# Kernel optimization log

Measured on AMD Instinct MI355X. Metric: run time of the kernel, lower is better.

## Reference

```python
import jax, jax.numpy as jnp
import numpy as np

B, C, H, W = 16, 192, 64, 64
L = 256           # number of quantization levels (len(sos.unique_values))
EXTREMA = 10.0    # codebook support roughly [-extrema, extrema]


def setup_inputs() -> dict:
    key = jax.random.key(0)
    k1, k2, k3 = jax.random.split(key, 3)
    inputs = jax.random.normal(k1, (B, C, H, W), dtype=jnp.float32) * 3.0
    means = jax.random.normal(k2, (B, C, H, W), dtype=jnp.float32)
    # sorted codebook of unique quantizer output values (sos.unique_values)
    raw = jax.random.uniform(k3, (L,), dtype=jnp.float32,
                             minval=-EXTREMA, maxval=EXTREMA)
    unique_values = jnp.sort(raw)
    return {"inputs": inputs, "means": means, "unique_values": unique_values}


def _nearest_symbols(v, unique_values):
    # Parallel binary search over the sorted codebook; equivalent to the
    # original per-element argmin(|keys - x|) in transform_map.
    L_ = unique_values.shape[0]
    idx = jnp.searchsorted(unique_values, v)          # in [0, L]
    idx = jnp.clip(idx, 1, L_ - 1)
    left = unique_values[idx - 1]
    right = unique_values[idx]
    # on ties, argmin picks the lower index -> use <=
    return jnp.where(jnp.abs(v - left) <= jnp.abs(v - right), idx - 1, idx)


def reference(inputs, means, unique_values):
    # quantize(mode='symbols'): subtract means, snap to nearest codebook
    # value, map value -> integer symbol via the sorted codebook.
    v = inputs - means
    symbols = _nearest_symbols(v, unique_values)      # int32 [B,C,H,W]
    # dequantize: symbol -> float codebook value (map_cdf_sos), add means.
    dequant = unique_values[symbols] + means          # float32 [B,C,H,W]
    return dequant, symbols
```

## Files before the change

### kernel.cpp

```cpp
#include <hip/hip_runtime.h>
#include <math.h>


#define LVL 256

__device__ __forceinline__ int lb_bj(const int* s_bj, int x) {
    int lo = 0, hi = LVL;
    #pragma unroll
    for (int s = 0; s < 8; ++s) {
        int mid = (lo + hi) >> 1;
        bool r = (s_bj[mid] < x);
        lo = r ? mid + 1 : lo;
        hi = r ? hi : mid;
    }
    return lo;
}

__global__ __launch_bounds__(256) void agc_build(
    const float* __restrict__ uv, float* __restrict__ ws, int NB)
{
    __shared__ float s_uv[LVL];
    __shared__ float s_mid[LVL];
    __shared__ int   s_bj[LVL];
    int tid = threadIdx.x;
    s_uv[tid] = uv[tid];
    __syncthreads();
    float mid = (tid < LVL - 1) ? 0.5f * (s_uv[tid] + s_uv[tid + 1]) : INFINITY;
    s_mid[tid] = mid;
    __syncthreads();
    float lo = s_mid[0], hi = s_mid[LVL - 2];
    float scale = (float)NB / (hi - lo);
    float f = (mid - lo) * scale;
    f = fminf(fmaxf(f, 0.0f), (float)(NB - 1));
    s_bj[tid] = (tid < LVL - 1) ? (int)f : 0x7fffffff;
    __syncthreads();

    if (blockIdx.x == 0) {
        float4 p;
        p.x = s_mid[tid];
        p.y = s_uv[tid];
        p.z = (tid < LVL - 1) ? s_uv[tid + 1] : s_uv[LVL - 1];
        p.w = 0.0f;
        ((float4*)ws)[tid] = p;
        if (tid == 0) { ws[1024] = lo; ws[1025] = scale; }
    }

    unsigned short* T = (unsigned short*)((char*)ws + 4608);
    int stride = gridDim.x * blockDim.x;
    for (int m = blockIdx.x * blockDim.x + tid; m < NB; m += stride) {
        int l0 = lb_bj(s_bj, m);
        int l1 = lb_bj(s_bj, m + 1);
        int cnt = l1 - l0;
        int base = l0 > 255 ? 255 : l0;
        int c = cnt > 2 ? 2 : cnt;
        T[m] = (unsigned short)(base | (c << 8));
    }
}

__device__ __forceinline__ int lb_mid(const float4* s_pack, float v) {
    int lo = 0, hi = LVL;
    #pragma unroll
    for (int s = 0; s < 8; ++s) {
        int mid = (lo + hi) >> 1;
        bool r = (s_pack[mid].x < v);
        lo = r ? mid + 1 : lo;
        hi = r ? hi : mid;
    }
    return lo;
}

__device__ __forceinline__ void agc_one4(
    const float4& a, const float4& b, const float4* s_pack,
    const unsigned short* __restrict__ T, float lo, float scale, float fNBm1,
    float4& dq, float4& sy)
{
    float v[4]  = {a.x - b.x, a.y - b.y, a.z - b.z, a.w - b.w};
    float me[4] = {b.x, b.y, b.z, b.w};
    float dqs[4], sys[4];
    int slow = 0;
    #pragma unroll
    for (int k = 0; k < 4; ++k) {
        float f = (v[k] - lo) * scale;
        f = fminf(fmaxf(f, 0.0f), fNBm1);
        int e = T[(int)f];
        int base = e & 255;
        int c = e >> 8;
        float4 p = s_pack[base];
        bool take = (c == 1) && (p.x < v[k]);
        sys[k] = (float)(base + (take ? 1 : 0));
        dqs[k] = (take ? p.z : p.y) + me[k];
        slow |= (c == 2) << k;
    }
    if (slow) {
        #pragma unroll
        for (int k = 0; k < 4; ++k) if ((slow >> k) & 1) {
            int s = lb_mid(s_pack, v[k]);
            sys[k] = (float)s;
            dqs[k] = s_pack[s].y + me[k];
        }
    }
    dq = make_float4(dqs[0], dqs[1], dqs[2], dqs[3]);
    sy = make_float4(sys[0], sys[1], sys[2], sys[3]);
}

__global__ __launch_bounds__(256) void agc_quant(
    const float* __restrict__ inputs, const float* __restrict__ means,
    const float* __restrict__ ws, const unsigned short* __restrict__ T,
    float* __restrict__ out_deq, float* __restrict__ out_sym,
    int n4, int n, int NB)
{
    __shared__ float4 s_pack[LVL];
    int tid = threadIdx.x;
    s_pack[tid] = ((const float4*)ws)[tid];
    float lo = ws[1024], scale = ws[1025];
    __syncthreads();

    const float4* in4 = (const float4*)inputs;
    const float4* mn4 = (const float4*)means;
    float4* dq4 = (float4*)out_deq;
    float4* sy4 = (float4*)out_sym;
    float fNBm1 = (float)(NB - 1);

    int i0 = blockIdx.x * 512 + tid;
    int i1 = i0 + 256;

    if (i1 < n4) {
        float4 a0 = in4[i0], b0 = mn4[i0], a1 = in4[i1], b1 = mn4[i1];
        float4 dq0, sy0, dq1, sy1;
        agc_one4(a0, b0, s_pack, T, lo, scale, fNBm1, dq0, sy0);
        agc_one4(a1, b1, s_pack, T, lo, scale, fNBm1, dq1, sy1);
        dq4[i0] = dq0; dq4[i1] = dq1;
        sy4[i0] = sy0; sy4[i1] = sy1;
    } else {
        if (i0 < n4) {
            float4 a = in4[i0], b = mn4[i0], dq, sy;
            agc_one4(a, b, s_pack, T, lo, scale, fNBm1, dq, sy);
            dq4[i0] = dq; sy4[i0] = sy;
        }
        if (i1 < n4) {
            float4 a = in4[i1], b = mn4[i1], dq, sy;
            agc_one4(a, b, s_pack, T, lo, scale, fNBm1, dq, sy);
            dq4[i1] = dq; sy4[i1] = sy;
        }
    }

    if (blockIdx.x == 0 && tid == 0) {
        for (int j = n4 * 4; j < n; ++j) {
            float m = means[j];
            float v = inputs[j] - m;
            int s = lb_mid(s_pack, v);
            out_sym[j] = (float)s;
            out_deq[j] = s_pack[s].y + m;
        }
    }
}

extern "C" void kernel_launch(void* const* d_in, const int* in_sizes, int n_in,
                              void* d_out, int out_size, void* d_ws, size_t ws_size,
                              hipStream_t stream) {
    const float* inputs = (const float*)d_in[0];
    const float* means  = (const float*)d_in[1];
    const float* uv     = (const float*)d_in[2];

    int n  = in_sizes[0];
    int n4 = n / 4;

    float* out     = (float*)d_out;
    float* out_deq = out;
    float* out_sym = out + n;
    float* ws      = (float*)d_ws;

    long long avail = (long long)ws_size > 4608 ? ((long long)ws_size - 4608) / 2 : 1024;
    int NB = 1024;
    while ((long long)NB * 2 <= avail && NB < 32768) NB <<= 1;
    unsigned short* T = (unsigned short*)((char*)d_ws + 4608);

    agc_build<<<32, 256, 0, stream>>>(uv, ws, NB);

    int blocks = (n4 + 511) / 512;
    agc_quant<<<blocks, 256, 0, stream>>>(
        inputs, means, ws, T, out_deq, out_sym, n4, n, NB);
}
```

Measured before the change: 220.1 us.

## Stage fat float4 bucket table in LDS and use persistent grid-stride blocks

Replaces the global ushort bucket table (up to 32K entries, read through cache) with a fixed 2048-entry table of float4 entries. Each entry holds the midpoint, both candidate codebook values and the base/count metadata, and every block copies it into LDS. The common case then needs a single LDS read per element instead of a global table read plus an LDS read, and buckets covering several levels walk the codebook linearly instead of running a binary search. The quant kernel becomes a persistent grid of 1024 blocks with a grid-stride loop, which amortises the 36KB LDS fill. The cost is lower occupancy from the larger LDS footprint and coarser buckets, so more elements take the multi-step path.

```diff
diff --git a/kernel.cpp b/kernel.cpp
--- a/kernel.cpp
+++ b/kernel.cpp
@@ -3,6 +3,7 @@
 
 
 #define LVL 256
+#define NB  2048
 
 __device__ __forceinline__ int lb_bj(const int* s_bj, int x) {
     int lo = 0, hi = LVL;
@@ -17,7 +18,7 @@
 }
 
 __global__ __launch_bounds__(256) void agc_build(
-    const float* __restrict__ uv, float* __restrict__ ws, int NB)
+    const float* __restrict__ uv, float* __restrict__ ws)
 {
     __shared__ float s_uv[LVL];
     __shared__ float s_mid[LVL];
@@ -42,18 +43,22 @@
         p.z = (tid < LVL - 1) ? s_uv[tid + 1] : s_uv[LVL - 1];
         p.w = 0.0f;
         ((float4*)ws)[tid] = p;
-        if (tid == 0) { ws[1024] = lo; ws[1025] = scale; }
+        if (tid == 0) { ws[9216] = lo; ws[9217] = scale; }
     }
 
-    unsigned short* T = (unsigned short*)((char*)ws + 4608);
+    float4* T = (float4*)(ws + 1024);
     int stride = gridDim.x * blockDim.x;
     for (int m = blockIdx.x * blockDim.x + tid; m < NB; m += stride) {
         int l0 = lb_bj(s_bj, m);
         int l1 = lb_bj(s_bj, m + 1);
         int cnt = l1 - l0;
-        int base = l0 > 255 ? 255 : l0;
-        int c = cnt > 2 ? 2 : cnt;
-        T[m] = (unsigned short)(base | (c << 8));
+        int b = l0 > 255 ? 255 : l0;
+        float4 e;
+        e.x = s_mid[b];
+        e.y = s_uv[b];
+        e.z = (b < LVL - 1) ? s_uv[b + 1] : s_uv[LVL - 1];
+        e.w = __int_as_float(b | (cnt << 16));
+        T[m] = e;
     }
 }
 
@@ -69,86 +74,94 @@
     return lo;
 }
 
-__device__ __forceinline__ void agc_one4(
-    const float4& a, const float4& b, const float4* s_pack,
-    const unsigned short* __restrict__ T, float lo, float scale, float fNBm1,
-    float4& dq, float4& sy)
-{
-    float v[4]  = {a.x - b.x, a.y - b.y, a.z - b.z, a.w - b.w};
-    float me[4] = {b.x, b.y, b.z, b.w};
-    float dqs[4], sys[4];
-    int slow = 0;
-    #pragma unroll
-    for (int k = 0; k < 4; ++k) {
-        float f = (v[k] - lo) * scale;
-        f = fminf(fmaxf(f, 0.0f), fNBm1);
-        int e = T[(int)f];
-        int base = e & 255;
-        int c = e >> 8;
-        float4 p = s_pack[base];
-        bool take = (c == 1) && (p.x < v[k]);
-        sys[k] = (float)(base + (take ? 1 : 0));
-        dqs[k] = (take ? p.z : p.y) + me[k];
-        slow |= (c == 2) << k;
-    }
-    if (slow) {
-        #pragma unroll
-        for (int k = 0; k < 4; ++k) if ((slow >> k) & 1) {
-            int s = lb_mid(s_pack, v[k]);
-            sys[k] = (float)s;
-            dqs[k] = s_pack[s].y + me[k];
-        }
-    }
-    dq = make_float4(dqs[0], dqs[1], dqs[2], dqs[3]);
-    sy = make_float4(sys[0], sys[1], sys[2], sys[3]);
-}
-
 __global__ __launch_bounds__(256) void agc_quant(
     const float* __restrict__ inputs, const float* __restrict__ means,
-    const float* __restrict__ ws, const unsigned short* __restrict__ T,
+    const float* __restrict__ ws,
     float* __restrict__ out_deq, float* __restrict__ out_sym,
-    int n4, int n, int NB)
+    int n4, int n)
 {
+    __shared__ float4 s_T[NB];
     __shared__ float4 s_pack[LVL];
     int tid = threadIdx.x;
+    const float4* gT = (const float4*)(ws + 1024);
+    #pragma unroll
+    for (int m = tid; m < NB; m += 256) s_T[m] = gT[m];
     s_pack[tid] = ((const float4*)ws)[tid];
-    float lo = ws[1024], scale = ws[1025];
+    float lo = ws[9216], scale = ws[9217];
     __syncthreads();
 
     const float4* in4 = (const float4*)inputs;
     const float4* mn4 = (const float4*)means;
     float4* dq4 = (float4*)out_deq;
     float4* sy4 = (float4*)out_sym;
-    float fNBm1 = (float)(NB - 1);
+    const float fNBm1 = (float)(NB - 1);
 
-    int i0 = blockIdx.x * 512 + tid;
-    int i1 = i0 + 256;
+    int nth = gridDim.x * blockDim.x;
+    int gid = blockIdx.x * blockDim.x + tid;
 
-    if (i1 < n4) {
-        float4 a0 = in4[i0], b0 = mn4[i0], a1 = in4[i1], b1 = mn4[i1];
-        float4 dq0, sy0, dq1, sy1;
-        agc_one4(a0, b0, s_pack, T, lo, scale, fNBm1, dq0, sy0);
-        agc_one4(a1, b1, s_pack, T, lo, scale, fNBm1, dq1, sy1);
-        dq4[i0] = dq0; dq4[i1] = dq1;
-        sy4[i0] = sy0; sy4[i1] = sy1;
-    } else {
-        if (i0 < n4) {
-            float4 a = in4[i0], b = mn4[i0], dq, sy;
-            agc_one4(a, b, s_pack, T, lo, scale, fNBm1, dq, sy);
-            dq4[i0] = dq; sy4[i0] = sy;
+    for (int base_i = gid; base_i < n4; base_i += 2 * nth) {
+        int i0 = base_i;
+        int i1 = base_i + nth;
+        bool h1 = (i1 < n4);
+
+        float4 a0 = in4[i0], b0 = mn4[i0];
+        float4 a1 = make_float4(0, 0, 0, 0), b1 = make_float4(0, 0, 0, 0);
+        if (h1) { a1 = in4[i1]; b1 = mn4[i1]; }
+
+        float v[8], me[8];
+        v[0] = a0.x - b0.x; v[1] = a0.y - b0.y; v[2] = a0.z - b0.z; v[3] = a0.w - b0.w;
+        v[4] = a1.x - b1.x; v[5] = a1.y - b1.y; v[6] = a1.z - b1.z; v[7] = a1.w - b1.w;
+        me[0] = b0.x; me[1] = b0.y; me[2] = b0.z; me[3] = b0.w;
+        me[4] = b1.x; me[5] = b1.y; me[6] = b1.z; me[7] = b1.w;
+
+        float4 t[8];
+        #pragma unroll
+        for (int k = 0; k < 8; ++k) {
+            float f = (v[k] - lo) * scale;
+            f = fminf(fmaxf(f, 0.0f), fNBm1);
+            t[k] = s_T[(int)f];
         }
-        if (i1 < n4) {
-            float4 a = in4[i1], b = mn4[i1], dq, sy;
-            agc_one4(a, b, s_pack, T, lo, scale, fNBm1, dq, sy);
-            dq4[i1] = dq; sy4[i1] = sy;
+
+        float dq[8], sy[8];
+        #pragma unroll
+        for (int k = 0; k < 8; ++k) {
+            int meta = __float_as_int(t[k].w);
+            int b   = meta & 0xffff;
+            int cnt = meta >> 16;
+            bool take1 = (cnt > 0) && (t[k].x < v[k]);
+            int   sym = b + (take1 ? 1 : 0);
+            float val = take1 ? t[k].z : t[k].y;
+            if (take1 && cnt >= 2) {
+                float4 p = s_pack[b + 1];
+                bool take2 = (p.x < v[k]);
+                sym += take2 ? 1 : 0;
+                val  = take2 ? p.z : val;
+                int kk = 2;
+                while (take2 && kk < cnt) {
+                    float4 p2 = s_pack[b + kk];
+                    take2 = (p2.x < v[k]);
+                    sym += take2 ? 1 : 0;
+                    val  = take2 ? p2.z : val;
+                    ++kk;
+                }
+            }
+            sy[k] = (float)sym;
+            dq[k] = val + me[k];
+        }
+
+        dq4[i0] = make_float4(dq[0], dq[1], dq[2], dq[3]);
+        sy4[i0] = make_float4(sy[0], sy[1], sy[2], sy[3]);
+        if (h1) {
+            dq4[i1] = make_float4(dq[4], dq[5], dq[6], dq[7]);
+            sy4[i1] = make_float4(sy[4], sy[5], sy[6], sy[7]);
         }
     }
 
     if (blockIdx.x == 0 && tid == 0) {
         for (int j = n4 * 4; j < n; ++j) {
             float m = means[j];
-            float v = inputs[j] - m;
-            int s = lb_mid(s_pack, v);
+            float vv = inputs[j] - m;
+            int s = lb_mid(s_pack, vv);
             out_sym[j] = (float)s;
             out_deq[j] = s_pack[s].y + m;
         }
@@ -170,14 +183,8 @@
     float* out_sym = out + n;
     float* ws      = (float*)d_ws;
 
-    long long avail = (long long)ws_size > 4608 ? ((long long)ws_size - 4608) / 2 : 1024;
-    int NB = 1024;
-    while ((long long)NB * 2 <= avail && NB < 32768) NB <<= 1;
-    unsigned short* T = (unsigned short*)((char*)d_ws + 4608);
+    agc_build<<<16, 256, 0, stream>>>(uv, ws);
 
-    agc_build<<<32, 256, 0, stream>>>(uv, ws, NB);
-
-    int blocks = (n4 + 511) / 512;
-    agc_quant<<<blocks, 256, 0, stream>>>(
-        inputs, means, ws, T, out_deq, out_sym, n4, n, NB);
+    agc_quant<<<1024, 256, 0, stream>>>(
+        inputs, means, ws, out_deq, out_sym, n4, n);
 }
```

Result: faster. 187.9 us (-14.6%).
